# Performance work log

Measured on AMD Instinct MI355X. Metric: run time of the kernel, lower is better.

Reference implementation:

```python
import jax, jax.numpy as jnp
import numpy as np

N_HEADS = 4
DIM_HEAD = 32
SCALE = DIM_HEAD ** -0.5
EPS = 1e-5


def setup_inputs() -> dict:
    key = jax.random.key(0)
    ks = jax.random.split(key, 5)
    b, dim, l, h, w = 8, 128, 32, 32, 32
    hidden = N_HEADS * DIM_HEAD  # 128
    return {
        "x": jax.random.normal(ks[0], (b, dim, l, h, w), dtype=jnp.float32),
        "w_qkv": jax.random.normal(ks[1], (3 * hidden, dim), dtype=jnp.float32) * 0.05,
        "w_out": jax.random.normal(ks[2], (dim, hidden), dtype=jnp.float32) * 0.05,
        "b_out": jax.random.normal(ks[3], (dim,), dtype=jnp.float32) * 0.05,
        "gn_gamma": jnp.ones((dim,), dtype=jnp.float32),
        "gn_beta": jnp.zeros((dim,), dtype=jnp.float32),
    }


def reference(x, w_qkv, w_out, b_out, gn_gamma, gn_beta):
    b, dim, l, h_sp, w_sp = x.shape
    n = l * h_sp * w_sp
    hidden = N_HEADS * DIM_HEAD
    xf = x.reshape(b, dim, n)  # flatten spatial -> tokens
    # 1x1 conv == channel matmul: [3*hidden, dim] x [b, dim, n]
    qkv = jnp.einsum('oc,bcn->bon', w_qkv, xf)
    qkv = qkv.reshape(b, 3, N_HEADS, DIM_HEAD, n)
    q, k, v = qkv[:, 0], qkv[:, 1], qkv[:, 2]  # each [b, H, d, n]
    q = jax.nn.softmax(q, axis=2) * SCALE      # softmax over feature dim d
    k = jax.nn.softmax(k, axis=-1)             # softmax over tokens n
    c = jnp.einsum('bhdn,bhen->bhde', k, v)    # [b, H, d, e] tiny context
    out = jnp.einsum('bhde,bhdn->bhen', c, q)  # [b, H, e, n]
    out = out.reshape(b, hidden, n)
    # to_out 1x1 conv + bias
    y = jnp.einsum('oc,bcn->bon', w_out, out) + b_out[None, :, None]
    # GroupNorm(1, dim): normalize over (C, spatial) per sample
    mean = jnp.mean(y, axis=(1, 2), keepdims=True)
    var = jnp.var(y, axis=(1, 2), keepdims=True)
    y = (y - mean) * jax.lax.rsqrt(var + EPS)
    y = y * gn_gamma[None, :, None] + gn_beta[None, :, None]
    return y.reshape(b, dim, l, h_sp, w_sp)
```

## Files before the change

kernel.cpp:

```cpp
#include <hip/hip_runtime.h>

#define BATCH 8
#define DIMC 128
#define NTOT 32768
#define HEADS 4
#define DHEAD 32
#define SCALE_Q 0.17677669529663687f
#define GRIDX 64
#define TILES 8

typedef _Float16 half8  __attribute__((ext_vector_type(8)));
typedef _Float16 half4v __attribute__((ext_vector_type(4)));
typedef float    f32x4  __attribute__((ext_vector_type(4)));

#define WS_WQKV 0
#define WS_S    98304
#define WS_Z    229376
#define WS_ST   233472
#define WS_GOFF 0
#define WS_NEED 299072


__global__ void k0_prep(const float* __restrict__ wqkv, char* __restrict__ ws) {
    int i = blockIdx.x * 256 + threadIdx.x;
    _Float16* Wb = (_Float16*)(ws + WS_WQKV);
    float* S  = (float*)(ws + WS_S);
    float* Z  = (float*)(ws + WS_Z);
    float* St = (float*)(ws + WS_ST);
    if (i < 49152) Wb[i] = (_Float16)wqkv[i];
    int j = i - 49152;
    if (j >= 0 && j < 32768) S[j] = 0.f;
    int k = j - 32768;
    if (k >= 0 && k < 1024) Z[k] = 0.f;
    int m = k - 1024;
    if (m >= 0 && m < 16) St[m] = 0.f;
}

__global__ __launch_bounds__(256, 1) void k1_kv(const float* __restrict__ x,
                                                const _Float16* __restrict__ Wb,
                                                float* __restrict__ S,
                                                float* __restrict__ Z,
                                                char* __restrict__ ybase) {
    __shared__ _Float16 Xb[64][136];
    __shared__ _Float16 KB[128][64];
    __shared__ _Float16 VB[128][64];
    __shared__ _Float16 EQ[128][64];
    const int t = threadIdx.x;
    const int lane = t & 63, w = t >> 6, g = lane >> 4, l15 = lane & 15;
    const int b = blockIdx.y;

    half8 wa[2][4];
#pragma unroll
    for (int mi = 0; mi < 2; ++mi)
#pragma unroll
        for (int kc = 0; kc < 4; ++kc)
            wa[mi][kc] = *(const half8*)(Wb + (size_t)((w * 2 + mi) * 16 + l15) * 128 + kc * 32 + 8 * g);

    half8 vone;
#pragma unroll
    for (int i = 0; i < 8; ++i) vone[i] = (_Float16)1.0f;

    f32x4 sacc[2][2];
#pragma unroll
    for (int dm = 0; dm < 2; ++dm)
#pragma unroll
        for (int en = 0; en < 2; ++en) sacc[dm][en] = (f32x4){0.f, 0.f, 0.f, 0.f};
    f32x4 zacc[2];
    zacc[0] = (f32x4){0.f, 0.f, 0.f, 0.f};
    zacc[1] = (f32x4){0.f, 0.f, 0.f, 0.f};

    const int j4 = t & 15, c0 = t >> 4;
    const int sxw = (j4 & 7) << 3;

    float4 xr[8];
#pragma unroll
    for (int cc = 0; cc < 8; ++cc)
        xr[cc] = *(const float4*)(x + ((size_t)b * DIMC + c0 + 16 * cc) * NTOT + blockIdx.x * 64 + 4 * j4);
#pragma unroll
    for (int cc = 0; cc < 8; ++cc) {
        const int c = c0 + 16 * cc;
        Xb[4 * j4 + 0][c ^ sxw] = (_Float16)xr[cc].x;
        Xb[4 * j4 + 1][c ^ sxw] = (_Float16)xr[cc].y;
        Xb[4 * j4 + 2][c ^ sxw] = (_Float16)xr[cc].z;
        Xb[4 * j4 + 3][c ^ sxw] = (_Float16)xr[cc].w;
    }

    for (int it = 0; it < TILES; ++it) {
        const int j0 = (blockIdx.x + GRIDX * it) * 64;
        __syncthreads();
        half8 bf[4][4];
#pragma unroll
        for (int nt = 0; nt < 4; ++nt) {
            const int sb = ((4 * nt + (l15 >> 2)) & 7) << 3;
#pragma unroll
            for (int kc = 0; kc < 4; ++kc)
                bf[nt][kc] = *(const half8*)(&Xb[nt * 16 + l15][(kc * 32 + 8 * g) ^ sb]);
        }
        {
            f32x4 eacc[2][4];
#pragma unroll
            for (int mi = 0; mi < 2; ++mi)
#pragma unroll
                for (int nt = 0; nt < 4; ++nt) eacc[mi][nt] = (f32x4){0.f, 0.f, 0.f, 0.f};
#pragma unroll
            for (int mi = 0; mi < 2; ++mi)
#pragma unroll
                for (int kc = 0; kc < 4; ++kc)
#pragma unroll
                    for (int nt = 0; nt < 4; ++nt)
                        eacc[mi][nt] = __builtin_amdgcn_mfma_f32_16x16x32_f16(wa[mi][kc], bf[nt][kc], eacc[mi][nt], 0, 0, 0);
            float ps[4] = {0.f, 0.f, 0.f, 0.f};
#pragma unroll
            for (int mi = 0; mi < 2; ++mi)
#pragma unroll
                for (int nt = 0; nt < 4; ++nt)
#pragma unroll
                    for (int r = 0; r < 4; ++r) {
                        const float e = __expf(eacc[mi][nt][r]);
                        ps[nt] += e;
                        eacc[mi][nt][r] = e;
                    }
            float scn[4];
#pragma unroll
            for (int nt = 0; nt < 4; ++nt) {
                ps[nt] += __shfl_xor(ps[nt], 16);
                ps[nt] += __shfl_xor(ps[nt], 32);
                scn[nt] = SCALE_Q / ps[nt];
            }
#pragma unroll
            for (int mi = 0; mi < 2; ++mi) {
                const int d0 = (w * 2 + mi) * 16 + g * 4;
                const int sq = (((w * 2 + mi) * 4 + g) & 7) << 3;
#pragma unroll
                for (int nt = 0; nt < 4; ++nt) {
                    const int jn = (nt * 16 + l15) ^ sq;
#pragma unroll
                    for (int r = 0; r < 4; ++r)
                        EQ[d0 + r][jn] = (_Float16)(eacc[mi][nt][r] * scn[nt]);
                }
            }
        }
        if (it < TILES - 1) {
            const int j0n = (blockIdx.x + GRIDX * (it + 1)) * 64;
#pragma unroll
            for (int cc = 0; cc < 8; ++cc)
                xr[cc] = *(const float4*)(x + ((size_t)b * DIMC + c0 + 16 * cc) * NTOT + j0n + 4 * j4);
        }
#pragma unroll
        for (int mt = 0; mt < 4; ++mt) {
            half8 afm[4];
#pragma unroll
            for (int kc = 0; kc < 4; ++kc)
                afm[kc] = *(const half8*)(Wb + (size_t)(128 + (w * 4 + mt) * 16 + l15) * 128 + kc * 32 + 8 * g);
            f32x4 a0 = (f32x4){0.f,0.f,0.f,0.f}, a1 = a0, a2 = a0, a3 = a0;
#pragma unroll
            for (int kc = 0; kc < 4; ++kc) {
                a0 = __builtin_amdgcn_mfma_f32_16x16x32_f16(bf[0][kc], afm[kc], a0, 0, 0, 0);
                a1 = __builtin_amdgcn_mfma_f32_16x16x32_f16(bf[1][kc], afm[kc], a1, 0, 0, 0);
                a2 = __builtin_amdgcn_mfma_f32_16x16x32_f16(bf[2][kc], afm[kc], a2, 0, 0, 0);
                a3 = __builtin_amdgcn_mfma_f32_16x16x32_f16(bf[3][kc], afm[kc], a3, 0, 0, 0);
            }
            const int row16 = (w * 4 + mt) * 16;
            const int sk = ((mt * 4 + (l15 >> 2)) & 7) << 3;
            if (row16 < 128) {
#pragma unroll
                for (int jt = 0; jt < 4; ++jt) {
                    const f32x4 a = (jt == 0) ? a0 : (jt == 1) ? a1 : (jt == 2) ? a2 : a3;
                    half4v p;
#pragma unroll
                    for (int r = 0; r < 4; ++r) p[r] = (_Float16)__expf(a[r]);
                    *(half4v*)(&KB[row16 + l15][(jt * 16 + g * 4) ^ sk]) = p;
                }
            } else {
#pragma unroll
                for (int jt = 0; jt < 4; ++jt) {
                    const f32x4 a = (jt == 0) ? a0 : (jt == 1) ? a1 : (jt == 2) ? a2 : a3;
                    half4v p;
#pragma unroll
                    for (int r = 0; r < 4; ++r) p[r] = (_Float16)a[r];
                    *(half4v*)(&VB[row16 - 128 + l15][(jt * 16 + g * 4) ^ sk]) = p;
                }
            }
        }
        __syncthreads();
        if (it < TILES - 1) {
#pragma unroll
            for (int cc = 0; cc < 8; ++cc) {
                const int c = c0 + 16 * cc;
                Xb[4 * j4 + 0][c ^ sxw] = (_Float16)xr[cc].x;
                Xb[4 * j4 + 1][c ^ sxw] = (_Float16)xr[cc].y;
                Xb[4 * j4 + 2][c ^ sxw] = (_Float16)xr[cc].z;
                Xb[4 * j4 + 3][c ^ sxw] = (_Float16)xr[cc].w;
            }
        }
#pragma unroll
        for (int dm = 0; dm < 2; ++dm) {
            const int sr = ((4 * dm + (l15 >> 2)) & 7) << 3;
            half8 ka0 = *(const half8*)(&KB[w * 32 + dm * 16 + l15][(8 * g) ^ sr]);
            half8 ka1 = *(const half8*)(&KB[w * 32 + dm * 16 + l15][(32 + 8 * g) ^ sr]);
            zacc[dm] = __builtin_amdgcn_mfma_f32_16x16x32_f16(ka0, vone, zacc[dm], 0, 0, 0);
            zacc[dm] = __builtin_amdgcn_mfma_f32_16x16x32_f16(ka1, vone, zacc[dm], 0, 0, 0);
#pragma unroll
            for (int en = 0; en < 2; ++en) {
                const int se = ((4 * en + (l15 >> 2)) & 7) << 3;
                half8 vb0 = *(const half8*)(&VB[w * 32 + en * 16 + l15][(8 * g) ^ se]);
                half8 vb1 = *(const half8*)(&VB[w * 32 + en * 16 + l15][(32 + 8 * g) ^ se]);
                sacc[dm][en] = __builtin_amdgcn_mfma_f32_16x16x32_f16(ka0, vb0, sacc[dm][en], 0, 0, 0);
                sacc[dm][en] = __builtin_amdgcn_mfma_f32_16x16x32_f16(ka1, vb1, sacc[dm][en], 0, 0, 0);
            }
        }
#pragma unroll
        for (int p = 0; p < 4; ++p) {
            const int idx = p * 256 + t, d = idx >> 3, c8 = idx & 7;
            half8 v = *(const half8*)(&EQ[d][(c8 * 8) ^ ((((d) >> 2) & 7) << 3)]);
            *(half8*)((_Float16*)(ybase + (size_t)(b * DIMC + d) * 131072) + j0 + c8 * 8) = v;
        }
    }
    if (l15 == 0) {
#pragma unroll
        for (int dm = 0; dm < 2; ++dm)
#pragma unroll
            for (int r = 0; r < 4; ++r)
                atomicAdd(&Z[(b * HEADS + w) * DHEAD + dm * 16 + g * 4 + r], zacc[dm][r]);
    }
#pragma unroll
    for (int dm = 0; dm < 2; ++dm)
#pragma unroll
        for (int en = 0; en < 2; ++en)
#pragma unroll
            for (int r = 0; r < 4; ++r)
                atomicAdd(&S[((size_t)(b * HEADS + w) * DHEAD + dm * 16 + g * 4 + r) * DHEAD + en * 16 + l15],
                          sacc[dm][en][r]);
}

__global__ __launch_bounds__(256) void k2_g(const float* __restrict__ S, const float* __restrict__ Z,
                                            const float* __restrict__ wout, _Float16* __restrict__ G) {
    __shared__ float Sd[32][33];
    const int h = blockIdx.x, b = blockIdx.y;
    const int t = threadIdx.x;
    const float* Sb = S + (size_t)(b * HEADS + h) * 1024;
    const float* Zb = Z + (size_t)(b * HEADS + h) * 32;
    for (int i = t; i < 1024; i += 256) {
        int d = i >> 5;
        Sd[d][i & 31] = Sb[i] / Zb[d];
    }
    __syncthreads();
    const int o = t & 127, dh = (t >> 7) * 16;
    float wrow[32];
#pragma unroll
    for (int e = 0; e < 32; ++e) wrow[e] = wout[o * 128 + h * 32 + e];
    _Float16* Gb = G + (size_t)b * 16384;
#pragma unroll
    for (int dd = 0; dd < 16; ++dd) {
        const int d = dh + dd;
        float acc = 0.f;
#pragma unroll
        for (int e = 0; e < 32; ++e) acc = fmaf(wrow[e], Sd[d][e], acc);
        Gb[o * 128 + h * 32 + d] = (_Float16)acc;
    }
}

__global__ __launch_bounds__(256, 2) void k3_main(const _Float16* __restrict__ G,
                                                  const float* __restrict__ b_out,
                                                  char* __restrict__ ybase,
                                                  float* __restrict__ St) {
    __shared__ _Float16 EB[64][136];
    __shared__ float red[8];
    const int t = threadIdx.x;
    const int lane = t & 63, w = t >> 6, g = lane >> 4, l15 = lane & 15;
    const int b = blockIdx.y;

    half8 ga[2][4];
    float bo[2][4];
    const _Float16* Gb = G + (size_t)b * 16384;
#pragma unroll
    for (int mi = 0; mi < 2; ++mi) {
        const int o = (w * 2 + mi) * 16 + l15;
#pragma unroll
        for (int kc = 0; kc < 4; ++kc)
            ga[mi][kc] = *(const half8*)(Gb + (size_t)o * 128 + kc * 32 + 8 * g);
#pragma unroll
        for (int r = 0; r < 4; ++r) bo[mi][r] = b_out[(w * 2 + mi) * 16 + g * 4 + r];
    }

    float ssum = 0.f, ssq = 0.f;
    half8 er[4];

#pragma unroll
    for (int p = 0; p < 4; ++p) {
        const int idx = p * 256 + t, d = idx >> 3, jj = (idx & 7) * 8;
        er[p] = *(const half8*)((const _Float16*)(ybase + (size_t)(b * DIMC + d) * 131072) + blockIdx.x * 64 + jj);
    }
#pragma unroll
    for (int p = 0; p < 4; ++p) {
        const int idx = p * 256 + t, d = idx >> 3, jj = (idx & 7) * 8;
#pragma unroll
        for (int e = 0; e < 8; ++e) EB[jj + e][d ^ ((((jj + e) >> 2) & 7) << 3)] = er[p][e];
    }
    __syncthreads();

    for (int it = 0; it < TILES; ++it) {
        const int j0 = (blockIdx.x + GRIDX * it) * 64;
        if (it < TILES - 1) {
            const int j0n = (blockIdx.x + GRIDX * (it + 1)) * 64;
#pragma unroll
            for (int p = 0; p < 4; ++p) {
                const int idx = p * 256 + t, d = idx >> 3, jj = (idx & 7) * 8;
                er[p] = *(const half8*)((const _Float16*)(ybase + (size_t)(b * DIMC + d) * 131072) + j0n + jj);
            }
        }
        {
            half8 bf[4][4];
#pragma unroll
            for (int nt = 0; nt < 4; ++nt) {
                const int sb = ((4 * nt + (l15 >> 2)) & 7) << 3;
#pragma unroll
                for (int kc = 0; kc < 4; ++kc)
                    bf[nt][kc] = *(const half8*)(&EB[nt * 16 + l15][(kc * 32 + 8 * g) ^ sb]);
            }
#pragma unroll
            for (int mi = 0; mi < 2; ++mi) {
                const int o0 = (w * 2 + mi) * 16 + g * 4;
                f32x4 acc[4];
#pragma unroll
                for (int nt = 0; nt < 4; ++nt) acc[nt] = (f32x4){0.f, 0.f, 0.f, 0.f};
#pragma unroll
                for (int kc = 0; kc < 4; ++kc)
#pragma unroll
                    for (int nt = 0; nt < 4; ++nt)
                        acc[nt] = __builtin_amdgcn_mfma_f32_16x16x32_f16(ga[mi][kc], bf[nt][kc], acc[nt], 0, 0, 0);
#pragma unroll
                for (int r = 0; r < 4; ++r) {
                    _Float16* yrow = (_Float16*)(ybase + (size_t)(b * DIMC + o0 + r) * 131072 + 65536);
#pragma unroll
                    for (int nt = 0; nt < 4; ++nt) {
                        const float yv = acc[nt][r] + bo[mi][r];
                        ssum += yv;
                        ssq += yv * yv;
                        yrow[j0 + nt * 16 + l15] = (_Float16)yv;
                    }
                }
            }
        }
        __syncthreads();
        if (it < TILES - 1) {
#pragma unroll
            for (int p = 0; p < 4; ++p) {
                const int idx = p * 256 + t, d = idx >> 3, jj = (idx & 7) * 8;
#pragma unroll
                for (int e = 0; e < 8; ++e) EB[jj + e][d ^ ((((jj + e) >> 2) & 7) << 3)] = er[p][e];
            }
        }
        __syncthreads();
    }
#pragma unroll
    for (int m = 32; m; m >>= 1) { ssum += __shfl_xor(ssum, m); ssq += __shfl_xor(ssq, m); }
    if (lane == 0) { red[w] = ssum; red[4 + w] = ssq; }
    __syncthreads();
    if (t == 0) {
        atomicAdd(&St[b * 2 + 0], red[0] + red[1] + red[2] + red[3]);
        atomicAdd(&St[b * 2 + 1], red[4] + red[5] + red[6] + red[7]);
    }
}

__global__ __launch_bounds__(256) void k4_norm(float* __restrict__ out, const float* __restrict__ St,
                                               const float* __restrict__ gamma,
                                               const float* __restrict__ beta) {
    const int o = blockIdx.x;
    const int b = blockIdx.y;
    const int t = threadIdx.x;
    const size_t row = (size_t)b * DIMC + o;
    const float n = (float)DIMC * (float)NTOT;
    const float mean = St[b * 2] / n;
    const float var = St[b * 2 + 1] / n - mean * mean;
    const float rs = rsqrtf(var + 1e-5f);
    const float ga = gamma[o] * rs;
    const float be = beta[o];
    const half8* yh = (const half8*)((const char*)out + row * 131072 + 65536);
    half8 hbuf[16];
#pragma unroll
    for (int i = 0; i < 16; ++i) hbuf[i] = yh[i * 256 + t];
    __syncthreads();
    float4* orow = (float4*)(out + row * NTOT);
#pragma unroll
    for (int i = 0; i < 16; ++i) {
        const int e4 = (i * 256 + t) * 2;
        float4 v0, v1;
        v0.x = ((float)hbuf[i][0] - mean) * ga + be;
        v0.y = ((float)hbuf[i][1] - mean) * ga + be;
        v0.z = ((float)hbuf[i][2] - mean) * ga + be;
        v0.w = ((float)hbuf[i][3] - mean) * ga + be;
        v1.x = ((float)hbuf[i][4] - mean) * ga + be;
        v1.y = ((float)hbuf[i][5] - mean) * ga + be;
        v1.z = ((float)hbuf[i][6] - mean) * ga + be;
        v1.w = ((float)hbuf[i][7] - mean) * ga + be;
        orow[e4] = v0;
        orow[e4 + 1] = v1;
    }
}

extern "C" void kernel_launch(void* const* d_in, const int* in_sizes, int n_in,
                              void* d_out, int out_size, void* d_ws, size_t ws_size,
                              hipStream_t stream) {
    const float* x     = (const float*)d_in[0];
    const float* wqkv  = (const float*)d_in[1];
    const float* wout  = (const float*)d_in[2];
    const float* b_out = (const float*)d_in[3];
    const float* gamma = (const float*)d_in[4];
    const float* beta  = (const float*)d_in[5];
    if (ws_size < WS_NEED) return;
    char* ws = (char*)d_ws;
    _Float16* Wb = (_Float16*)(ws + WS_WQKV);
    float* S  = (float*)(ws + WS_S);
    float* Z  = (float*)(ws + WS_Z);
    float* St = (float*)(ws + WS_ST);
    _Float16* G = (_Float16*)(ws + WS_GOFF);

    k0_prep<<<325, 256, 0, stream>>>(wqkv, ws);
    k1_kv<<<dim3(GRIDX, 8), 256, 0, stream>>>(x, Wb, S, Z, (char*)d_out);
    k2_g<<<dim3(HEADS, 8), 256, 0, stream>>>(S, Z, wout, G);
    k3_main<<<dim3(GRIDX, 8), 256, 0, stream>>>(G, b_out, (char*)d_out, St);
    k4_norm<<<dim3(128, 8), 256, 0, stream>>>((float*)d_out, St, gamma, beta);
}
```

Measured before the change: 159.1 us.

## Store softmaxed Q token-major in scratch and hoist fixed K/V weight fragments

The intermediate Q tile in the workspace is now stored token-major, with 128 channels contiguous per token, instead of channel-major. Both the producer (k1) and the consumer (k3) can then move it with contiguous half8 accesses, which removes the scalar 8-element scatter into shared memory in k3. The K/V weight fragments are also loaded once into registers before the tile loop instead of on every tile, at the cost of more register pressure. The workspace layout changes, so k3's addressing must match k1's exactly.

Result: no change. 156.9 us (-1.4%).

```diff
diff --git a/kernel.cpp b/kernel.cpp
--- a/kernel.cpp
+++ b/kernel.cpp
@@ -44,17 +44,23 @@
     __shared__ _Float16 Xb[64][136];
     __shared__ _Float16 KB[128][64];
     __shared__ _Float16 VB[128][64];
-    __shared__ _Float16 EQ[128][64];
+    __shared__ _Float16 EQT[64][136];
     const int t = threadIdx.x;
     const int lane = t & 63, w = t >> 6, g = lane >> 4, l15 = lane & 15;
     const int b = blockIdx.y;
 
     half8 wa[2][4];
+    half8 af[4][4];
 #pragma unroll
     for (int mi = 0; mi < 2; ++mi)
 #pragma unroll
         for (int kc = 0; kc < 4; ++kc)
             wa[mi][kc] = *(const half8*)(Wb + (size_t)((w * 2 + mi) * 16 + l15) * 128 + kc * 32 + 8 * g);
+#pragma unroll
+    for (int mt = 0; mt < 4; ++mt)
+#pragma unroll
+        for (int kc = 0; kc < 4; ++kc)
+            af[mt][kc] = *(const half8*)(Wb + (size_t)(128 + (w * 4 + mt) * 16 + l15) * 128 + kc * 32 + 8 * g);
 
     half8 vone;
 #pragma unroll
@@ -128,17 +134,14 @@
                 scn[nt] = SCALE_Q / ps[nt];
             }
 #pragma unroll
-            for (int mi = 0; mi < 2; ++mi) {
-                const int d0 = (w * 2 + mi) * 16 + g * 4;
-                const int sq = (((w * 2 + mi) * 4 + g) & 7) << 3;
+            for (int mi = 0; mi < 2; ++mi)
 #pragma unroll
                 for (int nt = 0; nt < 4; ++nt) {
-                    const int jn = (nt * 16 + l15) ^ sq;
-#pragma unroll
-                    for (int r = 0; r < 4; ++r)
-                        EQ[d0 + r][jn] = (_Float16)(eacc[mi][nt][r] * scn[nt]);
+                    half4v p;
+#pragma unroll
+                    for (int r = 0; r < 4; ++r) p[r] = (_Float16)(eacc[mi][nt][r] * scn[nt]);
+                    *(half4v*)(&EQT[nt * 16 + l15][(w * 2 + mi) * 16 + g * 4]) = p;
                 }
-            }
         }
         if (it < TILES - 1) {
             const int j0n = (blockIdx.x + GRIDX * (it + 1)) * 64;
@@ -148,17 +151,13 @@
         }
 #pragma unroll
         for (int mt = 0; mt < 4; ++mt) {
-            half8 afm[4];
-#pragma unroll
-            for (int kc = 0; kc < 4; ++kc)
-                afm[kc] = *(const half8*)(Wb + (size_t)(128 + (w * 4 + mt) * 16 + l15) * 128 + kc * 32 + 8 * g);
             f32x4 a0 = (f32x4){0.f,0.f,0.f,0.f}, a1 = a0, a2 = a0, a3 = a0;
 #pragma unroll
             for (int kc = 0; kc < 4; ++kc) {
-                a0 = __builtin_amdgcn_mfma_f32_16x16x32_f16(bf[0][kc], afm[kc], a0, 0, 0, 0);
-                a1 = __builtin_amdgcn_mfma_f32_16x16x32_f16(bf[1][kc], afm[kc], a1, 0, 0, 0);
-                a2 = __builtin_amdgcn_mfma_f32_16x16x32_f16(bf[2][kc], afm[kc], a2, 0, 0, 0);
-                a3 = __builtin_amdgcn_mfma_f32_16x16x32_f16(bf[3][kc], afm[kc], a3, 0, 0, 0);
+                a0 = __builtin_amdgcn_mfma_f32_16x16x32_f16(bf[0][kc], af[mt][kc], a0, 0, 0, 0);
+                a1 = __builtin_amdgcn_mfma_f32_16x16x32_f16(bf[1][kc], af[mt][kc], a1, 0, 0, 0);
+                a2 = __builtin_amdgcn_mfma_f32_16x16x32_f16(bf[2][kc], af[mt][kc], a2, 0, 0, 0);
+                a3 = __builtin_amdgcn_mfma_f32_16x16x32_f16(bf[3][kc], af[mt][kc], a3, 0, 0, 0);
             }
             const int row16 = (w * 4 + mt) * 16;
             const int sk = ((mt * 4 + (l15 >> 2)) & 7) << 3;
@@ -209,11 +208,14 @@
                 sacc[dm][en] = __builtin_amdgcn_mfma_f32_16x16x32_f16(ka1, vb1, sacc[dm][en], 0, 0, 0);
             }
         }
-#pragma unroll
-        for (int p = 0; p < 4; ++p) {
-            const int idx = p * 256 + t, d = idx >> 3, c8 = idx & 7;
-            half8 v = *(const half8*)(&EQ[d][(c8 * 8) ^ ((((d) >> 2) & 7) << 3)]);
-            *(half8*)((_Float16*)(ybase + (size_t)(b * DIMC + d) * 131072) + j0 + c8 * 8) = v;
+        {
+            char* tb = ybase + (size_t)(b * DIMC + (j0 >> 8)) * 131072 + (size_t)(j0 & 255) * 256;
+#pragma unroll
+            for (int p = 0; p < 4; ++p) {
+                const int idx = p * 256 + t, jl = idx >> 4, d0 = (idx & 15) * 8;
+                half8 v = *(const half8*)(&EQT[jl][d0]);
+                *(half8*)(tb + (size_t)jl * 256 + d0 * 2) = v;
+            }
         }
     }
     if (l15 == 0) {
@@ -286,27 +288,31 @@
     float ssum = 0.f, ssq = 0.f;
     half8 er[4];
 
-#pragma unroll
-    for (int p = 0; p < 4; ++p) {
-        const int idx = p * 256 + t, d = idx >> 3, jj = (idx & 7) * 8;
-        er[p] = *(const half8*)((const _Float16*)(ybase + (size_t)(b * DIMC + d) * 131072) + blockIdx.x * 64 + jj);
-    }
-#pragma unroll
-    for (int p = 0; p < 4; ++p) {
-        const int idx = p * 256 + t, d = idx >> 3, jj = (idx & 7) * 8;
-#pragma unroll
-        for (int e = 0; e < 8; ++e) EB[jj + e][d ^ ((((jj + e) >> 2) & 7) << 3)] = er[p][e];
+    {
+        const int jb = blockIdx.x * 64;
+        const char* tb = ybase + (size_t)(b * DIMC + (jb >> 8)) * 131072 + (size_t)(jb & 255) * 256;
+#pragma unroll
+        for (int p = 0; p < 4; ++p) {
+            const int idx = p * 256 + t, jl = idx >> 4, d0 = (idx & 15) * 8;
+            er[p] = *(const half8*)(tb + (size_t)jl * 256 + d0 * 2);
+        }
+#pragma unroll
+        for (int p = 0; p < 4; ++p) {
+            const int idx = p * 256 + t, jl = idx >> 4, d0 = (idx & 15) * 8;
+            *(half8*)(&EB[jl][d0 ^ (((jl >> 2) & 7) << 3)]) = er[p];
+        }
     }
     __syncthreads();
 
     for (int it = 0; it < TILES; ++it) {
         const int j0 = (blockIdx.x + GRIDX * it) * 64;
         if (it < TILES - 1) {
-            const int j0n = (blockIdx.x + GRIDX * (it + 1)) * 64;
+            const int jn = (blockIdx.x + GRIDX * (it + 1)) * 64;
+            const char* tb = ybase + (size_t)(b * DIMC + (jn >> 8)) * 131072 + (size_t)(jn & 255) * 256;
 #pragma unroll
             for (int p = 0; p < 4; ++p) {
-                const int idx = p * 256 + t, d = idx >> 3, jj = (idx & 7) * 8;
-                er[p] = *(const half8*)((const _Float16*)(ybase + (size_t)(b * DIMC + d) * 131072) + j0n + jj);
+                const int idx = p * 256 + t, jl = idx >> 4, d0 = (idx & 15) * 8;
+                er[p] = *(const half8*)(tb + (size_t)jl * 256 + d0 * 2);
             }
         }
         {
@@ -346,9 +352,8 @@
         if (it < TILES - 1) {
 #pragma unroll
             for (int p = 0; p < 4; ++p) {
-                const int idx = p * 256 + t, d = idx >> 3, jj = (idx & 7) * 8;
-#pragma unroll
-                for (int e = 0; e < 8; ++e) EB[jj + e][d ^ ((((jj + e) >> 2) & 7) << 3)] = er[p][e];
+                const int idx = p * 256 + t, jl = idx >> 4, d0 = (idx & 15) * 8;
+                *(half8*)(&EB[jl][d0 ^ (((jl >> 2) & 7) << 3)]) = er[p];
             }
         }
         __syncthreads();
```
